# Kernel tuning notes

Measured on AMD Instinct MI355X. Metric: run time of the kernel, lower is better.

Reference implementation:

```python
import jax, jax.numpy as jnp
import numpy as np

D_MODEL = 1024
HEADS = 16
D_K = D_MODEL // HEADS
THETA = 10000.0


def _rope(x, pos):
    # x: [B, H, S, d_k]; pos: [S]
    half = D_K // 2
    inv_freq = 1.0 / (THETA ** (jnp.arange(0, D_K, 2, dtype=jnp.float32) / D_K))  # [half]
    ang = pos.astype(jnp.float32)[:, None] * inv_freq[None, :]  # [S, half]
    cos, sin = jnp.cos(ang), jnp.sin(ang)
    x1 = x[..., 0::2]  # even components
    x2 = x[..., 1::2]  # odd components
    o1 = x1 * cos - x2 * sin
    o2 = x1 * sin + x2 * cos
    # interleave back to original layout
    out = jnp.stack([o1, o2], axis=-1).reshape(x.shape)
    return out


def setup_inputs() -> dict:
    key = jax.random.key(0)
    ks = jax.random.split(key, 5)
    B, S = 4, 2048
    scale = 1.0 / np.sqrt(D_MODEL)
    return {
        "x": jax.random.normal(ks[0], (B, S, D_MODEL), dtype=jnp.float32),
        "Wq": jax.random.normal(ks[1], (D_MODEL, D_MODEL), dtype=jnp.float32) * scale,
        "Wk": jax.random.normal(ks[2], (D_MODEL, D_MODEL), dtype=jnp.float32) * scale,
        "Wv": jax.random.normal(ks[3], (D_MODEL, D_MODEL), dtype=jnp.float32) * scale,
        "Wo": jax.random.normal(ks[4], (D_MODEL, D_MODEL), dtype=jnp.float32) * scale,
    }


def reference(x, Wq, Wk, Wv, Wo):
    B, S, _ = x.shape
    # Linear weights are [out, in]; y = x @ W.T
    def proj(W):
        y = jnp.einsum('bsd,ed->bse', x, W)
        return y.reshape(B, S, HEADS, D_K).transpose(0, 2, 1, 3)  # [B,H,S,d_k]
    Q, K, V = proj(Wq), proj(Wk), proj(Wv)
    pos = jnp.arange(S, dtype=jnp.int32)
    Q = _rope(Q, pos)
    K = _rope(K, pos)
    scores = jnp.einsum('bhqd,bhkd->bhqk', Q, K) / jnp.sqrt(jnp.float32(D_K))
    causal = jnp.tril(jnp.ones((S, S), dtype=bool))
    scores = jnp.where(causal, scores, jnp.finfo(scores.dtype).min)
    attn = jax.nn.softmax(scores, axis=-1)
    mh = jnp.einsum('bhqk,bhkd->bhqd', attn, V)  # [B,H,S,d_v]
    mh = mh.transpose(0, 2, 1, 3).reshape(B, S, D_MODEL)
    return jnp.einsum('bsd,ed->bse', mh, Wo)
```

## Files before the change

kernel.cpp:

```cpp
#include <hip/hip_runtime.h>

typedef unsigned short u16;
typedef unsigned int   u32;
typedef __attribute__((ext_vector_type(8))) short s16x8;
typedef __attribute__((ext_vector_type(4))) float f32x4;
typedef __attribute__((ext_vector_type(16))) float f32x16;
typedef __attribute__((ext_vector_type(2))) int i32x2;

#define D_MODEL 1024
#define S_LEN   2048
#define BATCH   4
#define HEADS   16
#define DK      64
#define M_TOTAL (BATCH * S_LEN)

#define QSCALE 0.18033688011112042f
#define ROPE_L2 0.41524101186092029f

__device__ __forceinline__ u16 f2b(float f) {
  u32 u = __float_as_uint(f);
  u32 r = u + 0x7FFFu + ((u >> 16) & 1u);
  return (u16)(r >> 16);
}
__device__ __forceinline__ u32 packtrunc(float f0, float f1) {
  return (__float_as_uint(f0) >> 16) | (__float_as_uint(f1) & 0xFFFF0000u);
}
__device__ __forceinline__ u32 packrn(float f0, float f1) {
  return (u32)f2b(f0) | ((u32)f2b(f1) << 16);
}

extern "C" __device__ float __ocml_native_exp2_f32(float);
__device__ __forceinline__ float fexp2(float x) {
#if __has_builtin(__builtin_amdgcn_exp2f)
  return __builtin_amdgcn_exp2f(x);
#else
  return __ocml_native_exp2_f32(x);
#endif
}

typedef const __attribute__((address_space(1))) unsigned int* gas_u32p;
typedef __attribute__((address_space(3))) unsigned int* las_u32p;
#define GLL16(gp, lp) __builtin_amdgcn_global_load_lds((gas_u32p)(gp), (las_u32p)(lp), 16, 0, 0)

__global__ void k_f2bf(const float* __restrict__ in, u16* __restrict__ out, int n4) {
  int i = blockIdx.x * blockDim.x + threadIdx.x;
  if (i >= n4) return;
  float4 v = ((const float4*)in)[i];
  ((u32*)out)[2*i]   = packrn(v.x, v.y);
  ((u32*)out)[2*i+1] = packrn(v.z, v.w);
}

__global__ void k_f2bf4(const float* __restrict__ a, const float* __restrict__ b,
                        const float* __restrict__ c, const float* __restrict__ d,
                        u16* __restrict__ out) {
  int i = blockIdx.x * blockDim.x + threadIdx.x;
  const float* src = (i < 524288) ? ((i < 262144) ? a : b) : ((i < 786432) ? c : d);
  int off = i & 0x3FFFF;
  float4 v = ((const float4*)src)[off];
  ((u32*)out)[2*i]   = packrn(v.x, v.y);
  ((u32*)out)[2*i+1] = packrn(v.z, v.w);
}

template<bool BF16OUT, bool ROPE, bool DUAL>
__launch_bounds__(256, 4)
__global__ void k_gemm(const u16* __restrict__ A, const u16* __restrict__ B,
                       void* __restrict__ C, void* __restrict__ C2,
                       int M, int N, int K, float scale) {
  __shared__ u16 Al[128 * 32];
  __shared__ u16 Bl[128 * 32];
  const int tid  = threadIdx.x;
  const int lane = tid & 63;
  const int w    = tid >> 6;
  const int wm   = (w >> 1) * 64, wn = (w & 1) * 64;
  const int bm   = blockIdx.y * 128, bn = blockIdx.x * 128;
  const int row  = lane & 15, q = lane >> 4;

  f32x4 acc[4][4];
#pragma unroll
  for (int i = 0; i < 4; i++)
#pragma unroll
    for (int j = 0; j < 4; j++) acc[i][j] = (f32x4){0.f, 0.f, 0.f, 0.f};

  const int r16 = lane >> 2;
  const int cb  = (lane & 3) * 8;
  const u16* Ag0 = A + (size_t)(bm + w * 32 + r16) * K + cb;
  const u16* Ag1 = Ag0 + (size_t)16 * K;
  const u16* Bg0 = B + (size_t)(bn + w * 32 + r16) * K + cb;
  const u16* Bg1 = Bg0 + (size_t)16 * K;
  u16* Ad0 = Al + (w * 32) * 32;
  u16* Ad1 = Al + (w * 32 + 16) * 32;
  u16* Bd0 = Bl + (w * 32) * 32;
  u16* Bd1 = Bl + (w * 32 + 16) * 32;

  for (int k0 = 0; k0 < K; k0 += 32) {
    __syncthreads();
    GLL16(Ag0 + k0, Ad0);
    GLL16(Ag1 + k0, Ad1);
    GLL16(Bg0 + k0, Bd0);
    GLL16(Bg1 + k0, Bd1);
    __syncthreads();
    s16x8 af[4], bfr[4];
#pragma unroll
    for (int mi = 0; mi < 4; mi++)
      af[mi] = *(const s16x8*)(Al + (wm + mi * 16 + row) * 32 + q * 8);
#pragma unroll
    for (int ni = 0; ni < 4; ni++)
      bfr[ni] = *(const s16x8*)(Bl + (wn + ni * 16 + row) * 32 + q * 8);
#pragma unroll
    for (int mi = 0; mi < 4; mi++)
#pragma unroll
      for (int ni = 0; ni < 4; ni++)
        acc[mi][ni] = __builtin_amdgcn_mfma_f32_16x16x32_bf16(af[mi], bfr[ni], acc[mi][ni], 0, 0, 0);
  }

  const bool isQ = !DUAL || (bn < D_MODEL);
  u16* Cd = (u16*)(isQ ? C : C2);
  const int bnL = DUAL ? (bn & (D_MODEL - 1)) : bn;
  const float sc = isQ ? scale : 1.0f;

#pragma unroll
  for (int mi = 0; mi < 4; mi++)
#pragma unroll
    for (int ni = 0; ni < 4; ni++) {
      if (ROPE) {
        const int col = bnL + wn + ni * 16 + row;
        const int fi  = (col & 63) >> 1;
        const float inv = exp2f(-(float)fi * ROPE_L2);
        const bool odd = (row & 1);
#pragma unroll
        for (int r = 0; r < 4; r++) {
          int grow = bm + wm + mi * 16 + q * 4 + r;
          float own = acc[mi][ni][r];
          float oth = __shfl_xor(own, 1);
          float ang = (float)(grow & (S_LEN - 1)) * inv;
          float sn, cs;
          __sincosf(ang, &sn, &cs);
          float x1 = odd ? oth : own;
          float x2 = odd ? own : oth;
          float res = odd ? (x1 * sn + x2 * cs) : (x1 * cs - x2 * sn);
          acc[mi][ni][r] = res * sc;
        }
      }
#pragma unroll
      for (int r = 0; r < 4; r++) {
        int grow = bm + wm + mi * 16 + q * 4 + r;
        int gcol = bnL + wn + ni * 16 + row;
        float v = acc[mi][ni][r];
        if (BF16OUT) Cd[(size_t)grow * N + gcol] = f2b(v);
        else         ((float*)Cd)[(size_t)grow * N + gcol] = v;
      }
    }
}

__launch_bounds__(256, 4)
__global__ void k_attn(const u16* __restrict__ Qb, const u16* __restrict__ Kb,
                       const u16* __restrict__ Vtg, u16* __restrict__ Mh) {
  __shared__ u16 SH[128 * 64 + 64 * 128];
  u16* Kl = SH;
  u16* Vt = SH + 128 * 64;
  const int tid  = threadIdx.x;
  const int lane = tid & 63;
  const int w    = tid >> 6;
  const int n    = lane & 31;
  const int h    = lane >> 5;
  const int nx   = n & 7;
  const int bid = blockIdx.x;
  const int r   = bid >> 3;
  const int u   = r & 15;
  const int bh  = (bid & 7) + 8 * (r >> 4);
  const int hd  = bh & 15, b = bh >> 4;
  const int s   = (w & 2) ? (62 - 2 * u + (w & 1)) : (2 * u + (w & 1));
  const int rb  = s * 32;
  const int ktiles = ((63 - 2 * u) >> 2) + 1;
  const size_t kbase = ((size_t)b * S_LEN) * D_MODEL + (size_t)hd * DK;
  const size_t vbase = ((size_t)hd * DK) * M_TOTAL + (size_t)b * S_LEN;

  const int hx    = ((h ^ nx) << 3);
  const int kidx0 = n * 64  + hx;
  const int vidx0 = n * 128 + hx;

  s16x8 bq[4];
#pragma unroll
  for (int ks = 0; ks < 4; ks++)
    bq[ks] = *(const s16x8*)(Qb + kbase + (size_t)(rb + n) * D_MODEL + ks * 16 + h * 8);

  f32x16 o[2];
#pragma unroll
  for (int dt = 0; dt < 2; dt++)
#pragma unroll
    for (int i = 0; i < 16; i++) o[dt][i] = 0.f;
  float psum = 0.f;

  const int krow_l = lane >> 3;
  const int kblk_l = (lane & 7) ^ krow_l;
  const u16* KgL = Kb + kbase + (size_t)(w * 32 + krow_l) * D_MODEL + kblk_l * 8;
  u16* KdL = Kl + (w * 32) * 64;
  const int vrow_l = lane >> 4;
  const int vblk_l = lane & 15;
  const u16* VgL = Vtg + vbase + (size_t)(w * 16 + vrow_l) * M_TOTAL;
  u16* VdL = Vt + (w * 16) * 128;

  for (int t = 0; t < ktiles; t++) {
    const int k0 = t * 128;
    __syncthreads();
#pragma unroll
    for (int i = 0; i < 4; i++)
      GLL16(KgL + (size_t)(k0 + i * 8) * D_MODEL, KdL + i * 8 * 64);
#pragma unroll
    for (int i = 0; i < 4; i++) {
      const int jj = vblk_l ^ ((i * 4 + vrow_l) & 7);
      GLL16(VgL + (size_t)(i * 4) * M_TOTAL + k0 + jj * 8, VdL + i * 4 * 128);
    }
    __syncthreads();

#pragma unroll
    for (int kt = 0; kt < 4; kt++) {
      const int k0t = k0 + kt * 32;
      if (k0t > rb + 31) continue;

      s16x8 ak[4], vf[4];
#pragma unroll
      for (int ks = 0; ks < 4; ks++)
        ak[ks] = *(const s16x8*)(Kl + ((kidx0 ^ (ks << 4)) + kt * 2048));
#pragma unroll
      for (int c = 0; c < 2; c++)
#pragma unroll
        for (int dt = 0; dt < 2; dt++)
          vf[c * 2 + dt] = *(const s16x8*)(Vt + ((vidx0 ^ (kt * 32 + c * 16)) + dt * 4096));

      f32x16 Sc;
#pragma unroll
      for (int i = 0; i < 16; i++) Sc[i] = 0.f;
#pragma unroll
      for (int ks = 0; ks < 4; ks++)
        Sc = __builtin_amdgcn_mfma_f32_32x32x16_bf16(ak[ks], bq[ks], Sc, 0, 0, 0);

      u32 P0[4], P1[4];
      float ps01 = 0.f, ps23 = 0.f;
      if ((k0t + 31) > rb) {
        const int lim = rb + n - k0t - 4 * h;
#pragma unroll
        for (int g = 0; g < 4; g++) {
          float pv[4];
#pragma unroll
          for (int t2 = 0; t2 < 4; t2++) {
            float e = fexp2(Sc[4 * g + t2]);
            pv[t2] = (8 * g + t2 <= lim) ? e : 0.f;
          }
          ps01 += pv[0] + pv[1];
          ps23 += pv[2] + pv[3];
          P0[g] = packtrunc(pv[0], pv[1]);
          P1[g] = packtrunc(pv[2], pv[3]);
        }
      } else {
#pragma unroll
        for (int g = 0; g < 4; g++) {
          float pv[4];
#pragma unroll
          for (int t2 = 0; t2 < 4; t2++) pv[t2] = fexp2(Sc[4 * g + t2]);
          ps01 += pv[0] + pv[1];
          ps23 += pv[2] + pv[3];
          P0[g] = packtrunc(pv[0], pv[1]);
          P1[g] = packtrunc(pv[2], pv[3]);
        }
      }
      psum += ps01 + ps23;

#pragma unroll
      for (int c = 0; c < 2; c++) {
        i32x2 rA = __builtin_amdgcn_permlane32_swap((int)P0[2 * c], (int)P0[2 * c + 1], false, false);
        i32x2 rB = __builtin_amdgcn_permlane32_swap((int)P1[2 * c], (int)P1[2 * c + 1], false, false);
        union { u32 uu[4]; s16x8 v; } pb;
        pb.uu[0] = (u32)rA[0];
        pb.uu[1] = (u32)rB[0];
        pb.uu[2] = (u32)rA[1];
        pb.uu[3] = (u32)rB[1];
        o[0] = __builtin_amdgcn_mfma_f32_32x32x16_bf16(vf[c * 2 + 0], pb.v, o[0], 0, 0, 0);
        o[1] = __builtin_amdgcn_mfma_f32_32x32x16_bf16(vf[c * 2 + 1], pb.v, o[1], 0, 0, 0);
      }
    }
  }

  float l = psum + __shfl_xor(psum, 32);
  const float linv = 1.0f / l;
  __syncthreads();
  u16* Olw = SH + w * 32 * 66;
#pragma unroll
  for (int dt = 0; dt < 2; dt++) {
#pragma unroll
    for (int g = 0; g < 4; g++) {
      u32 lo = packrn(o[dt][4 * g + 0] * linv, o[dt][4 * g + 1] * linv);
      u32 hi = packrn(o[dt][4 * g + 2] * linv, o[dt][4 * g + 3] * linv);
      *(uint2*)(Olw + n * 66 + dt * 32 + 8 * g + 4 * h) = (uint2){lo, hi};
    }
  }
  const int rr = lane >> 3, seg = lane & 7;
#pragma unroll
  for (int ro = 0; ro < 32; ro += 8) {
    uint4 v = *(const uint4*)(Olw + (ro + rr) * 66 + seg * 8);
    *(uint4*)(Mh + ((size_t)b * S_LEN + rb + ro + rr) * D_MODEL + hd * DK + seg * 8) = v;
  }
}

extern "C" void kernel_launch(void* const* d_in, const int* in_sizes, int n_in,
                              void* d_out, int out_size, void* d_ws, size_t ws_size,
                              hipStream_t stream) {
  const float* x  = (const float*)d_in[0];
  const float* Wq = (const float*)d_in[1];
  const float* Wk = (const float*)d_in[2];
  const float* Wv = (const float*)d_in[3];
  const float* Wo = (const float*)d_in[4];
  float* out = (float*)d_out;

  char* ws = (char*)d_ws;
  const size_t xsz = (size_t)M_TOTAL * D_MODEL * 2;
  const size_t wsz = (size_t)D_MODEL * D_MODEL * 2;
  u16* Xb  = (u16*)ws; ws += xsz;
  u16* Wqb = (u16*)ws; ws += wsz;
  u16* Wkb = (u16*)ws; ws += wsz;
  u16* Wvb = (u16*)ws; ws += wsz;
  u16* Wob = (u16*)ws; ws += wsz;
  u16* Qb  = (u16*)ws; ws += xsz;
  u16* Kb  = (u16*)ws; ws += xsz;
  u16* Vtg = (u16*)ws; ws += xsz;
  u16* Mh  = (u16*)ws; ws += xsz;

  {
    int n4 = M_TOTAL * D_MODEL / 4;
    k_f2bf<<<(n4 + 255) / 256, 256, 0, stream>>>(x, Xb, n4);
    k_f2bf4<<<4096, 256, 0, stream>>>(Wq, Wk, Wv, Wo, Wqb);
  }

  dim3 gqk(2 * D_MODEL / 128, M_TOTAL / 128);
  k_gemm<true, true, true><<<gqk, 256, 0, stream>>>(Xb, Wqb, Qb, Kb, M_TOTAL, D_MODEL, D_MODEL, QSCALE);
  dim3 gv(M_TOTAL / 128, D_MODEL / 128);
  k_gemm<true, false, false><<<gv, 256, 0, stream>>>(Wvb, Xb, Vtg, Vtg, D_MODEL, M_TOTAL, D_MODEL, 1.0f);

  k_attn<<<dim3(1024), 256, 0, stream>>>(Qb, Kb, Vtg, Mh);

  dim3 gg(D_MODEL / 128, M_TOTAL / 128);
  k_gemm<false, false, false><<<gg, 256, 0, stream>>>(Mh, Wob, out, out, M_TOTAL, D_MODEL, D_MODEL, 1.0f);
}
```

Measured before the change: 259.6 us.

## Rewrite GEMM with larger tiles, 4-stage async LDS pipeline and swizzle

Replaces the 128x128 single-buffered GEMM with a templated kernel using 512 threads and larger block tiles (256x256, 128x256, 256x128). Global-to-LDS loads go into a 4-slot ring buffer, prefetched three tiles ahead and gated by explicit vmcnt waits, so memory latency overlaps the MFMA work. LDS rows are XOR-swizzled to avoid bank conflicts, and MFMA sections run at raised wave priority. Larger tiles raise register and LDS pressure and launch fewer blocks, which may underfill the GPU; the tail waitcnt logic must also match the outstanding-load counts exactly.

Result: no change. 258.6 us (-0.4%).

```diff
diff --git a/kernel.cpp b/kernel.cpp
--- a/kernel.cpp
+++ b/kernel.cpp
@@ -36,6 +36,10 @@
 #else
   return __ocml_native_exp2_f32(x);
 #endif
+}
+
+template<int N> __device__ __forceinline__ void waitvm() {
+  asm volatile("s_waitcnt vmcnt(%0)" :: "n"(N) : "memory");
 }
 
 typedef const __attribute__((address_space(1))) unsigned int* gas_u32p;
@@ -61,56 +65,88 @@
   ((u32*)out)[2*i+1] = packrn(v.z, v.w);
 }
 
-template<bool BF16OUT, bool ROPE, bool DUAL>
-__launch_bounds__(256, 4)
-__global__ void k_gemm(const u16* __restrict__ A, const u16* __restrict__ B,
-                       void* __restrict__ C, void* __restrict__ C2,
-                       int M, int N, int K, float scale) {
-  __shared__ u16 Al[128 * 32];
-  __shared__ u16 Bl[128 * 32];
+template<int BM, int BN, bool BF16OUT, bool ROPE, bool DUAL>
+__launch_bounds__(512, 2)
+__global__ void k_gemm2(const u16* __restrict__ A, const u16* __restrict__ B,
+                        void* __restrict__ C, void* __restrict__ C2,
+                        int M, int N, int K, float scale) {
+  constexpr int WM = BM / 2;
+  constexpr int WN = BN / 4;
+  constexpr int FM = WM / 16;
+  constexpr int FN = WN / 16;
+  constexpr int SA = BM / 128;
+  constexpr int SB = BN / 128;
+  constexpr int L  = SA + SB;
+  constexpr int ASLOT = BM * 32;
+  constexpr int SLOT  = (BM + BN) * 32;
+  __shared__ u16 SH[4 * SLOT];
+
   const int tid  = threadIdx.x;
   const int lane = tid & 63;
   const int w    = tid >> 6;
-  const int wm   = (w >> 1) * 64, wn = (w & 1) * 64;
-  const int bm   = blockIdx.y * 128, bn = blockIdx.x * 128;
-  const int row  = lane & 15, q = lane >> 4;
-
-  f32x4 acc[4][4];
-#pragma unroll
-  for (int i = 0; i < 4; i++)
-#pragma unroll
-    for (int j = 0; j < 4; j++) acc[i][j] = (f32x4){0.f, 0.f, 0.f, 0.f};
-
-  const int r16 = lane >> 2;
-  const int cb  = (lane & 3) * 8;
-  const u16* Ag0 = A + (size_t)(bm + w * 32 + r16) * K + cb;
-  const u16* Ag1 = Ag0 + (size_t)16 * K;
-  const u16* Bg0 = B + (size_t)(bn + w * 32 + r16) * K + cb;
-  const u16* Bg1 = Bg0 + (size_t)16 * K;
-  u16* Ad0 = Al + (w * 32) * 32;
-  u16* Ad1 = Al + (w * 32 + 16) * 32;
-  u16* Bd0 = Bl + (w * 32) * 32;
-  u16* Bd1 = Bl + (w * 32 + 16) * 32;
-
-  for (int k0 = 0; k0 < K; k0 += 32) {
-    __syncthreads();
-    GLL16(Ag0 + k0, Ad0);
-    GLL16(Ag1 + k0, Ad1);
-    GLL16(Bg0 + k0, Bd0);
-    GLL16(Bg1 + k0, Bd1);
-    __syncthreads();
-    s16x8 af[4], bfr[4];
-#pragma unroll
-    for (int mi = 0; mi < 4; mi++)
-      af[mi] = *(const s16x8*)(Al + (wm + mi * 16 + row) * 32 + q * 8);
-#pragma unroll
-    for (int ni = 0; ni < 4; ni++)
-      bfr[ni] = *(const s16x8*)(Bl + (wn + ni * 16 + row) * 32 + q * 8);
-#pragma unroll
-    for (int mi = 0; mi < 4; mi++)
-#pragma unroll
-      for (int ni = 0; ni < 4; ni++)
+  const int wm2  = w >> 2;
+  const int wn2  = w & 3;
+  const int rl   = lane & 15;
+  const int q    = lane >> 4;
+  const int bm = blockIdx.y * BM, bn = blockIdx.x * BN;
+
+  const int rowS = tid >> 2;
+  const int blkS = (tid & 3) ^ (rowS & 3);
+  const u16* Asrc = A + (size_t)(bm + rowS) * K + blkS * 8;
+  const u16* Bsrc = B + (size_t)(bn + rowS) * K + blkS * 8;
+  const int dstL = w * 512;
+
+  const int fbase = rl * 32 + ((q ^ (rl & 3)) * 8);
+  const int abase = wm2 * WM * 32 + fbase;
+  const int bbase = ASLOT + wn2 * WN * 32 + fbase;
+
+  f32x4 acc[FM][FN];
+#pragma unroll
+  for (int i = 0; i < FM; i++)
+#pragma unroll
+    for (int j = 0; j < FN; j++) acc[i][j] = (f32x4){0.f, 0.f, 0.f, 0.f};
+
+  const int nt = K >> 5;
+
+  auto STAGE = [&](int t) {
+    u16* slot = SH + (t & 3) * SLOT;
+    const int k0 = t << 5;
+#pragma unroll
+    for (int s = 0; s < SA; s++)
+      GLL16(Asrc + (size_t)(s * 128) * K + k0, slot + s * 4096 + dstL);
+#pragma unroll
+    for (int s = 0; s < SB; s++)
+      GLL16(Bsrc + (size_t)(s * 128) * K + k0, slot + ASLOT + s * 4096 + dstL);
+  };
+
+  STAGE(0); STAGE(1); STAGE(2);
+
+  for (int t = 0; t < nt; t++) {
+    if (t + 3 < nt) STAGE(t + 3);
+    const int rem = nt - 1 - t;
+    if (rem >= 3)      waitvm<3 * L>();
+    else if (rem == 2) waitvm<2 * L>();
+    else if (rem == 1) waitvm<L>();
+    else               waitvm<0>();
+    __builtin_amdgcn_s_barrier();
+
+    const u16* slot = SH + (t & 3) * SLOT;
+    s16x8 af[FM], bfr[FN];
+#pragma unroll
+    for (int mi = 0; mi < FM; mi++)
+      af[mi] = *(const s16x8*)(slot + abase + mi * 512);
+#pragma unroll
+    for (int ni = 0; ni < FN; ni++)
+      bfr[ni] = *(const s16x8*)(slot + bbase + ni * 512);
+
+    __builtin_amdgcn_s_setprio(1);
+#pragma unroll
+    for (int mi = 0; mi < FM; mi++)
+#pragma unroll
+      for (int ni = 0; ni < FN; ni++)
         acc[mi][ni] = __builtin_amdgcn_mfma_f32_16x16x32_bf16(af[mi], bfr[ni], acc[mi][ni], 0, 0, 0);
+    __builtin_amdgcn_s_setprio(0);
+    __builtin_amdgcn_s_barrier();
   }
 
   const bool isQ = !DUAL || (bn < D_MODEL);
@@ -119,17 +155,17 @@
   const float sc = isQ ? scale : 1.0f;
 
 #pragma unroll
-  for (int mi = 0; mi < 4; mi++)
-#pragma unroll
-    for (int ni = 0; ni < 4; ni++) {
+  for (int mi = 0; mi < FM; mi++)
+#pragma unroll
+    for (int ni = 0; ni < FN; ni++) {
       if (ROPE) {
-        const int col = bnL + wn + ni * 16 + row;
+        const int col = bnL + wn2 * WN + ni * 16 + rl;
         const int fi  = (col & 63) >> 1;
         const float inv = exp2f(-(float)fi * ROPE_L2);
-        const bool odd = (row & 1);
+        const bool odd = (rl & 1);
 #pragma unroll
         for (int r = 0; r < 4; r++) {
-          int grow = bm + wm + mi * 16 + q * 4 + r;
+          int grow = bm + wm2 * WM + mi * 16 + q * 4 + r;
           float own = acc[mi][ni][r];
           float oth = __shfl_xor(own, 1);
           float ang = (float)(grow & (S_LEN - 1)) * inv;
@@ -143,8 +179,8 @@
       }
 #pragma unroll
       for (int r = 0; r < 4; r++) {
-        int grow = bm + wm + mi * 16 + q * 4 + r;
-        int gcol = bnL + wn + ni * 16 + row;
+        int grow = bm + wm2 * WM + mi * 16 + q * 4 + r;
+        int gcol = bnL + wn2 * WN + ni * 16 + rl;
         float v = acc[mi][ni][r];
         if (BF16OUT) Cd[(size_t)grow * N + gcol] = f2b(v);
         else         ((float*)Cd)[(size_t)grow * N + gcol] = v;
@@ -331,13 +367,13 @@
     k_f2bf4<<<4096, 256, 0, stream>>>(Wq, Wk, Wv, Wo, Wqb);
   }
 
-  dim3 gqk(2 * D_MODEL / 128, M_TOTAL / 128);
-  k_gemm<true, true, true><<<gqk, 256, 0, stream>>>(Xb, Wqb, Qb, Kb, M_TOTAL, D_MODEL, D_MODEL, QSCALE);
-  dim3 gv(M_TOTAL / 128, D_MODEL / 128);
-  k_gemm<true, false, false><<<gv, 256, 0, stream>>>(Wvb, Xb, Vtg, Vtg, D_MODEL, M_TOTAL, D_MODEL, 1.0f);
+  k_gemm2<256, 256, true, true, true><<<dim3(8, 32), 512, 0, stream>>>(
+      Xb, Wqb, Qb, Kb, M_TOTAL, D_MODEL, D_MODEL, QSCALE);
+  k_gemm2<128, 256, true, false, false><<<dim3(32, 8), 512, 0, stream>>>(
+      Wvb, Xb, Vtg, Vtg, D_MODEL, M_TOTAL, D_MODEL, 1.0f);
 
   k_attn<<<dim3(1024), 256, 0, stream>>>(Qb, Kb, Vtg, Mh);
 
-  dim3 gg(D_MODEL / 128, M_TOTAL / 128);
-  k_gemm<false, false, false><<<gg, 256, 0, stream>>>(Mh, Wob, out, out, M_TOTAL, D_MODEL, D_MODEL, 1.0f);
-}
+  k_gemm2<256, 128, false, false, false><<<dim3(8, 32), 512, 0, stream>>>(
+      Mh, Wob, out, out, M_TOTAL, D_MODEL, D_MODEL, 1.0f);
+}
```
